# Kernel optimization log

Measured on AMD Instinct MI355X. Metric: run time of the kernel, lower is better.

Reference implementation:

```python
import jax, jax.numpy as jnp
import numpy as np

NC = 6            # CPAB tessellation cells (tess_size=6, zero_boundary=True)
DIM = NC - 1      # theta dimension = 5
SIG_LEN = 2048
CHANNELS = 3
BATCH = 256
FC_IN = 64 * 168  # flattened net_part1 output for signal_len=2048
NUM_SCALING = 0   # N in transform_data_ss
EPS_BN = 1e-5


def _cpab_basis():
    """QR null-space basis of the CPAB continuity + zero-boundary constraints.
    Params ordered [a_1,b_1,...,a_NC,b_NC]; v(x)=a_c x + b_c on cell c."""
    nc = NC
    L = np.zeros((nc + 1, 2 * nc))
    for k in range(1, nc):  # continuity at internal knots x_k = k/nc
        xk = k / nc
        L[k - 1, 2 * (k - 1)] = xk
        L[k - 1, 2 * (k - 1) + 1] = 1.0
        L[k - 1, 2 * k] = -xk
        L[k - 1, 2 * k + 1] = -1.0
    L[nc - 1, 1] = 1.0        # v(0) = 0  -> b_1 = 0
    L[nc, 2 * (nc - 1)] = 1.0  # v(1) = 0 -> a_nc + b_nc = 0
    L[nc, 2 * nc - 1] = 1.0
    Q, _ = np.linalg.qr(L.T, mode='complete')
    return np.ascontiguousarray(Q[:, nc + 1:]).astype(np.float32)  # (12, 5)


def _conv1d(x, w, b):
    y = jax.lax.conv_general_dilated(x, w, (1,), 'VALID',
                                     dimension_numbers=('NCH', 'OIH', 'NCH'))
    return y + b[None, :, None]


def _maxpool1d(x, k, s):
    return jax.lax.reduce_window(x, -jnp.inf, jax.lax.max, (1, 1, k), (1, 1, s), 'VALID')


def _bn(x, g, b, m, v):  # eval-mode BatchNorm1d
    return (x - m[None, :, None]) * (g / jnp.sqrt(v + EPS_BN))[None, :, None] + b[None, :, None]


def _integrate(x, A):
    """Exact CPAB 1D flow integration over t=1 with cell-crossing handling.
    x: (B, n) points in [0,1]; A: (B, NC, 2) per-cell (a, b). Monotone
    trajectories cross at most NC-1 boundaries -> fixed NC+1 iterations."""
    a_all, b_all = A[:, :, 0], A[:, :, 1]
    t = jnp.ones_like(x)
    for _ in range(NC + 1):
        c = jnp.clip(jnp.floor(x * NC).astype(jnp.int32), 0, NC - 1)
        a = jnp.take_along_axis(a_all, c, axis=1)
        b = jnp.take_along_axis(b_all, c, axis=1)
        v = a * x + b
        xb = jnp.where(v >= 0, (c + 1).astype(x.dtype) / NC, c.astype(x.dtype) / NC)
        big_a = jnp.abs(a) > 1e-8
        a_s = jnp.where(big_a, a, 1.0)
        z = x + b / a_s        # shifted coord: x(t) = z*exp(a t) - b/a
        zb = xb + b / a_s
        ratio = zb / jnp.where(jnp.abs(z) > 1e-12, z, 1e-12)
        t_exp = jnp.log(jnp.maximum(ratio, 1e-12)) / a_s
        v_s = jnp.where(jnp.abs(v) > 1e-12, v, 1.0)
        t_lin = (xb - x) / v_s
        thit = jnp.where(big_a, t_exp, t_lin)
        valid = (jnp.abs(v) > 1e-12) & (thit > 0) & (jnp.where(big_a, ratio, 1.0) > 0)
        thit = jnp.where(valid, thit, jnp.inf)
        tau = jnp.minimum(t, thit)
        x_new = jnp.where(big_a, z * jnp.exp(a * tau) - (z - x), x + b * tau)
        hit = thit <= t
        nudge = jnp.where(v >= 0, 1e-6, -1e-6)  # push into next cell
        x = jnp.clip(jnp.where(hit, xb + nudge, x_new), 0.0, 1.0)
        t = jnp.maximum(t - tau, 0.0)
    return x


def _interp1d(data, pos):
    """data: (B, L, C); pos: (B, n) in [0,1] -> (B, n, C) linear interpolation."""
    Lw = data.shape[1]
    p = jnp.clip(pos, 0.0, 1.0) * (Lw - 1)
    x0 = jnp.clip(jnp.floor(p).astype(jnp.int32), 0, Lw - 2)
    w = (p - x0.astype(p.dtype))[:, :, None]
    d0 = jnp.take_along_axis(data, x0[:, :, None], axis=1)
    d1 = jnp.take_along_axis(data, (x0 + 1)[:, :, None], axis=1)
    return d0 * (1.0 - w) + d1 * w


def _transform_data_ss(data, theta, basis, outsize, N):
    """CPAB scaling-and-squaring warp of data (B, L, C) by theta (B, DIM)."""
    Bsz = theta.shape[0]
    A = (theta @ basis.T).reshape(Bsz, NC, 2) / (2.0 ** N)
    grid = jnp.linspace(0.0, 1.0, outsize, dtype=data.dtype)
    grid_t = _integrate(jnp.broadcast_to(grid, (Bsz, outsize)), A)
    for _ in range(N):  # squaring: compose the warp with itself
        grid_t = _interp1d(grid_t[:, :, None], grid_t)[:, :, 0]
    return _interp1d(data, grid_t)


def reference(x, conv1_w, conv1_b, bn1_g, bn1_b, bn1_m, bn1_v,
              conv2_w, conv2_b, bn2_g, bn2_b, bn2_m, bn2_v,
              conv3_w, conv3_b, bn3_g, bn3_b, bn3_m, bn3_v,
              fc1_w, fc1_b, fc2_w, fc2_b, fc3_w, fc3_b, fc4_w, fc4_b, basis):
    # localization net (n_recurrence = 1, back_version = True)
    h = jax.nn.relu(_maxpool1d(_bn(_conv1d(x, conv1_w, conv1_b), bn1_g, bn1_b, bn1_m, bn1_v), 3, 2))
    h = jax.nn.relu(_maxpool1d(_bn(_conv1d(h, conv2_w, conv2_b), bn2_g, bn2_b, bn2_m, bn2_v), 3, 3))
    h = jax.nn.relu(_maxpool1d(_bn(_conv1d(h, conv3_w, conv3_b), bn3_g, bn3_b, bn3_m, bn3_v), 3, 2))
    xs = h.reshape(h.shape[0], -1)  # (B, 64*168)
    xs = jax.nn.relu(xs @ fc1_w.T + fc1_b)
    xs = jax.nn.relu(xs @ fc2_w.T + fc2_b)
    xs = jax.nn.relu(xs @ fc3_w.T + fc3_b)
    theta = jnp.tanh(xs @ fc4_w.T + fc4_b)  # (B, 5)
    data = jnp.transpose(x, (0, 2, 1))       # (B, L, C)
    warped = _transform_data_ss(data, theta, basis, SIG_LEN, NUM_SCALING)
    return jnp.transpose(warped, (0, 2, 1))  # (B, C, L)


def setup_inputs() -> dict:
    key = jax.random.key(0)
    ks = jax.random.split(key, 16)
    def nrm(k, shape, scale):
        return (jax.random.normal(k, shape) * scale).astype(jnp.float32)
    inp = {}
    inp['x'] = jax.random.normal(ks[0], (BATCH, CHANNELS, SIG_LEN), dtype=jnp.float32)
    inp['conv1_w'] = nrm(ks[1], (128, CHANNELS, 3), (CHANNELS * 3) ** -0.5)
    inp['conv1_b'] = nrm(ks[2], (128,), 0.01)
    inp['bn1_g'] = jnp.ones((128,), jnp.float32)
    inp['bn1_b'] = jnp.zeros((128,), jnp.float32)
    inp['bn1_m'] = nrm(ks[3], (128,), 0.1)
    inp['bn1_v'] = jnp.ones((128,), jnp.float32)
    inp['conv2_w'] = nrm(ks[4], (64, 128, 5), (128 * 5) ** -0.5)
    inp['conv2_b'] = nrm(ks[5], (64,), 0.01)
    inp['bn2_g'] = jnp.ones((64,), jnp.float32)
    inp['bn2_b'] = jnp.zeros((64,), jnp.float32)
    inp['bn2_m'] = nrm(ks[6], (64,), 0.1)
    inp['bn2_v'] = jnp.ones((64,), jnp.float32)
    inp['conv3_w'] = nrm(ks[7], (64, 64, 3), (64 * 3) ** -0.5)
    inp['conv3_b'] = nrm(ks[8], (64,), 0.01)
    inp['bn3_g'] = jnp.ones((64,), jnp.float32)
    inp['bn3_b'] = jnp.zeros((64,), jnp.float32)
    inp['bn3_m'] = nrm(ks[9], (64,), 0.1)
    inp['bn3_v'] = jnp.ones((64,), jnp.float32)
    inp['fc1_w'] = nrm(ks[10], (48, FC_IN), FC_IN ** -0.5)
    inp['fc1_b'] = jnp.zeros((48,), jnp.float32)
    inp['fc2_w'] = nrm(ks[11], (32, 48), 48 ** -0.5)
    inp['fc2_b'] = jnp.zeros((32,), jnp.float32)
    inp['fc3_w'] = nrm(ks[12], (16, 32), 32 ** -0.5)
    inp['fc3_b'] = jnp.zeros((16,), jnp.float32)
    # near-identity warp head (original zero-inits weight, identity bias)
    inp['fc4_w'] = nrm(ks[13], (DIM, 16), 0.01)
    inp['fc4_b'] = nrm(ks[14], (DIM,), 0.01)
    inp['basis'] = jnp.asarray(_cpab_basis())
    return inp
```

## Files before the change

### kernel.cpp

```cpp
#include <hip/hip_runtime.h>
#include <math.h>

#define BATCH   256
#define SIGLEN  2048
#define L1OUT   1022
#define L2OUT   339
#define L3OUT   168
#define FCIN    10752

#define TP2   21
#define NROW  68
#define H1S   136
#define H1SZ  (NROW*H1S)

#define TU3   28

#define KC1   12
#define KCL   (FCIN/KC1)

typedef float f32x4  __attribute__((ext_vector_type(4)));
typedef float f32x16 __attribute__((ext_vector_type(16)));
typedef short s16x8  __attribute__((ext_vector_type(8)));

__device__ __forceinline__ unsigned short f2bf(float f) {
    unsigned int u = __float_as_uint(f);
    return (unsigned short)((u + 0x7fffu + ((u >> 16) & 1u)) >> 16);
}
__device__ __forceinline__ float bf2f(unsigned short h) {
    return __uint_as_float(((unsigned int)h) << 16);
}

__launch_bounds__(256)
__global__ void prep_kernel(
    const float* __restrict__ conv1_b,
    const float* __restrict__ g1, const float* __restrict__ b1,
    const float* __restrict__ m1, const float* __restrict__ v1,
    const float* __restrict__ conv2_w, const float* __restrict__ conv2_b,
    const float* __restrict__ g2, const float* __restrict__ b2,
    const float* __restrict__ m2, const float* __restrict__ v2,
    const float* __restrict__ conv3_w, const float* __restrict__ conv3_b,
    const float* __restrict__ g3, const float* __restrict__ b3,
    const float* __restrict__ m3, const float* __restrict__ v3,
    unsigned short* __restrict__ w2hi, unsigned short* __restrict__ w2lo,
    unsigned short* __restrict__ w3hi, unsigned short* __restrict__ w3lo,
    float* __restrict__ so1, float* __restrict__ so2, float* __restrict__ so3)
{
    int tid = blockIdx.x * 256 + threadIdx.x;
    int stride = gridDim.x * 256;
    for (int i = tid; i < 64*128*5; i += stride) {
        int co = i / 640; int rr = i - co*640; int ci = rr / 5; int k = rr - ci*5;
        float w = conv2_w[i];
        unsigned short hi = f2bf(w);
        unsigned short lo = f2bf(w - bf2f(hi));
        int seg = k*8 + (ci >> 4);
        int dst = ((seg*2 + (co >> 5))*32 + (co & 31))*16 + (ci & 15);
        w2hi[dst] = hi;
        w2lo[dst] = lo;
    }
    for (int i = tid; i < 64*64*3; i += stride) {
        int co = i / 192; int r = i - co*192; int ci = r / 3; int k = r - ci*3;
        float w = conv3_w[i];
        unsigned short hi = f2bf(w);
        unsigned short lo = f2bf(w - bf2f(hi));
        int dst = ((k*2 + (ci >> 5))*64 + co)*32 + (ci & 31);
        w3hi[dst] = hi;
        w3lo[dst] = lo;
    }
    if (tid < 128) {
        float s = g1[tid] / sqrtf(v1[tid] + 1e-5f);
        so1[tid]       = s;
        so1[128 + tid] = (conv1_b[tid] - m1[tid]) * s + b1[tid];
    }
    if (tid < 64) {
        float s2 = g2[tid] / sqrtf(v2[tid] + 1e-5f);
        so2[tid]      = s2;
        so2[64 + tid] = (conv2_b[tid] - m2[tid]) * s2 + b2[tid];
        float s3 = g3[tid] / sqrtf(v3[tid] + 1e-5f);
        so3[tid]      = s3;
        so3[64 + tid] = (conv3_b[tid] - m3[tid]) * s3 + b3[tid];
    }
}

__launch_bounds__(256, 4)
__global__ void conv12_kernel(
    const float* __restrict__ x, const float* __restrict__ w1,
    const unsigned short* __restrict__ w2hi, const unsigned short* __restrict__ w2lo,
    const float* __restrict__ so1, const float* __restrict__ so2,
    unsigned int* __restrict__ h2p)
{
    __shared__ unsigned short h1s[2 * H1SZ];

    int t  = threadIdx.x;
    int b  = blockIdx.x;
    int u0 = blockIdx.y * TP2;
    int q0 = 3 * u0;
    int wv = __builtin_amdgcn_readfirstlane(t >> 6);
    int l  = t & 63;

    float wr[2][9];
    float s1r[2], o1r[2];
    #pragma unroll
    for (int h = 0; h < 2; ++h) {
        int ch = l + 64*h;
        #pragma unroll
        for (int j = 0; j < 9; ++j) wr[h][j] = w1[ch*9 + j];
        s1r[h] = so1[ch]; o1r[h] = so1[128 + ch];
    }
    for (int s = 0; s < 17; ++s) {
        int r = 4*s + wv;
        int xbase = 2*(q0 + r);
        float xv[3][5];
        #pragma unroll
        for (int ci = 0; ci < 3; ++ci) {
            const float* xp = x + (b*3 + ci)*SIGLEN;
            #pragma unroll
            for (int d = 0; d < 5; ++d) {
                int xi = xbase + d; xi = xi < SIGLEN ? xi : SIGLEN - 1;
                xv[ci][d] = xp[xi];
            }
        }
        #pragma unroll
        for (int h = 0; h < 2; ++h) {
            float r0 = 0.f, r1 = 0.f, r2 = 0.f;
            #pragma unroll
            for (int ci = 0; ci < 3; ++ci) {
                float wA = wr[h][ci*3], wB = wr[h][ci*3+1], wC = wr[h][ci*3+2];
                r0 = fmaf(xv[ci][0], wA, fmaf(xv[ci][1], wB, fmaf(xv[ci][2], wC, r0)));
                r1 = fmaf(xv[ci][1], wA, fmaf(xv[ci][2], wB, fmaf(xv[ci][3], wC, r1)));
                r2 = fmaf(xv[ci][2], wA, fmaf(xv[ci][3], wB, fmaf(xv[ci][4], wC, r2)));
            }
            float mx = fmaxf(r0, fmaxf(r1, r2));
            float v  = fmaxf(fmaf(s1r[h], mx, o1r[h]), 0.f);
            unsigned short hi = f2bf(v);
            unsigned short lo = f2bf(v - bf2f(hi));
            h1s[r*H1S + l + 64*h]        = hi;
            h1s[H1SZ + r*H1S + l + 64*h] = lo;
        }
    }
    __syncthreads();

    int chf = wv & 1;
    int kh  = wv >> 1;
    int r32 = l & 31;
    int oct = l >> 5;

    f32x16 acc0 = (f32x16)(0.f);
    f32x16 acc1 = (f32x16)(0.f);
    const unsigned short* whB = w2hi + (chf*32 + r32)*16 + oct*8;
    const unsigned short* wlB = w2lo + (chf*32 + r32)*16 + oct*8;

    #pragma unroll 4
    for (int ss = 0; ss < 20; ++ss) {
        int sg = kh*20 + ss;
        int ks = sg >> 3, cb = sg & 7;
        s16x8 wh = *(const s16x8*)(whB + sg*1024);
        s16x8 wl = *(const s16x8*)(wlB + sg*1024);
        int row0 = r32 + ks;
        int row1 = 32 + r32 + ks;
        s16x8 ah0 = *(const s16x8*)&h1s[row0*H1S + cb*16 + oct*8];
        s16x8 al0 = *(const s16x8*)&h1s[H1SZ + row0*H1S + cb*16 + oct*8];
        s16x8 ah1 = *(const s16x8*)&h1s[row1*H1S + cb*16 + oct*8];
        s16x8 al1 = *(const s16x8*)&h1s[H1SZ + row1*H1S + cb*16 + oct*8];
        acc0 = __builtin_amdgcn_mfma_f32_32x32x16_bf16(ah0, wh, acc0, 0, 0, 0);
        acc1 = __builtin_amdgcn_mfma_f32_32x32x16_bf16(ah1, wh, acc1, 0, 0, 0);
        acc0 = __builtin_amdgcn_mfma_f32_32x32x16_bf16(al0, wh, acc0, 0, 0, 0);
        acc1 = __builtin_amdgcn_mfma_f32_32x32x16_bf16(al1, wh, acc1, 0, 0, 0);
        acc0 = __builtin_amdgcn_mfma_f32_32x32x16_bf16(ah0, wl, acc0, 0, 0, 0);
        acc1 = __builtin_amdgcn_mfma_f32_32x32x16_bf16(ah1, wl, acc1, 0, 0, 0);
    }
    __syncthreads();

    float* c2 = (float*)h1s;
    #pragma unroll
    for (int rg = 0; rg < 16; ++rg) {
        int row = (rg & 3) + 8*(rg >> 2) + 4*oct;
        c2[kh*4160 + row*65        + chf*32 + r32] = acc0[rg];
        c2[kh*4160 + (32 + row)*65 + chf*32 + r32] = acc1[rg];
    }
    __syncthreads();

    #pragma unroll
    for (int it = 0; it < 6; ++it) {
        int idx = t + it*256;
        if (idx < TP2*64) {
            int ul = idx >> 6, co = idx & 63;
            int u = u0 + ul;
            if (u < L2OUT) {
                float v0 = c2[(3*ul  )*65 + co] + c2[4160 + (3*ul  )*65 + co];
                float v1 = c2[(3*ul+1)*65 + co] + c2[4160 + (3*ul+1)*65 + co];
                float v2 = c2[(3*ul+2)*65 + co] + c2[4160 + (3*ul+2)*65 + co];
                float mm = fmaxf(v0, fmaxf(v1, v2));
                float v  = fmaxf(fmaf(so2[co], mm, so2[64 + co]), 0.f);
                unsigned short hi = f2bf(v);
                unsigned short lo = f2bf(v - bf2f(hi));
                h2p[(b*L2OUT + u)*64 + co] = (unsigned int)hi | ((unsigned int)lo << 16);
            }
        }
    }
}

__launch_bounds__(256, 4)
__global__ void conv3_kernel(
    const unsigned int* __restrict__ h2p,
    const unsigned short* __restrict__ w3hi, const unsigned short* __restrict__ w3lo,
    const float* __restrict__ so3, float* __restrict__ xs)
{
    __shared__ unsigned short h3hi[66 * 72];
    __shared__ unsigned short h3lo[66 * 72];

    int t  = threadIdx.x;
    int b  = blockIdx.x;
    int u0 = blockIdx.y * TU3;
    int wv = __builtin_amdgcn_readfirstlane(t >> 6);
    int l  = t & 63;
    int m  = l & 15;
    int qd = l >> 4;

    for (int i = t; i < 66*64; i += 256) {
        int r = i >> 6, ci = i & 63;
        int g = 2*u0 + r; g = g > (L2OUT-1) ? (L2OUT-1) : g;
        unsigned int v = h2p[(b*L2OUT + g)*64 + ci];
        h3hi[r*72 + ci] = (unsigned short)(v & 0xffffu);
        h3lo[r*72 + ci] = (unsigned short)(v >> 16);
    }
    __syncthreads();

    s16x8 wh[6], wl[6];
    #pragma unroll
    for (int s = 0; s < 6; ++s) {
        wh[s] = *(const s16x8*)(w3hi + s*2048 + (wv*16 + m)*32 + qd*8);
        wl[s] = *(const s16x8*)(w3lo + s*2048 + (wv*16 + m)*32 + qd*8);
    }

    f32x4 acc[4] = {(f32x4)(0.f), (f32x4)(0.f), (f32x4)(0.f), (f32x4)(0.f)};
    #pragma unroll
    for (int pt = 0; pt < 4; ++pt) {
        #pragma unroll
        for (int s = 0; s < 6; ++s) {
            int row = pt*16 + m + (s >> 1);
            int off = (s & 1)*32 + qd*8;
            s16x8 ah = *(const s16x8*)&h3hi[row*72 + off];
            s16x8 al = *(const s16x8*)&h3lo[row*72 + off];
            acc[pt] = __builtin_amdgcn_mfma_f32_16x16x32_bf16(ah, wh[s], acc[pt], 0, 0, 0);
            acc[pt] = __builtin_amdgcn_mfma_f32_16x16x32_bf16(al, wh[s], acc[pt], 0, 0, 0);
            acc[pt] = __builtin_amdgcn_mfma_f32_16x16x32_bf16(ah, wl[s], acc[pt], 0, 0, 0);
        }
    }
    __syncthreads();

    float* c3 = (float*)h3hi;
    #pragma unroll
    for (int pt = 0; pt < 4; ++pt)
        #pragma unroll
        for (int rg = 0; rg < 4; ++rg)
            c3[(pt*16 + qd*4 + rg)*65 + wv*16 + m] = acc[pt][rg];
    __syncthreads();

    #pragma unroll
    for (int it = 0; it < 7; ++it) {
        int idx = t + it*256;
        if (idx < TU3*64) {
            int co = idx / TU3, ul = idx - co*TU3;
            int p = 2*ul;
            float v0 = c3[(p  )*65 + co];
            float v1 = c3[(p+1)*65 + co];
            float v2 = c3[(p+2)*65 + co];
            float mm = fmaxf(v0, fmaxf(v1, v2));
            xs[b*FCIN + co*L3OUT + (u0 + ul)] = fmaxf(fmaf(so3[co], mm, so3[64 + co]), 0.f);
        }
    }
}

__launch_bounds__(256)
__global__ void fc1_kernel(
    const float* __restrict__ xs, const float* __restrict__ w,
    float* __restrict__ part)
{
    int t = threadIdx.x, lane = t & 63, wid = t >> 6;
    int b0 = blockIdx.x * 4;
    int kc = blockIdx.y;
    int o0 = wid * 12;
    float acc[48];
    #pragma unroll
    for (int i = 0; i < 48; ++i) acc[i] = 0.f;

    int kbase = kc * KCL + lane;
    for (int ki = 0; ki < KCL/64; ++ki) {
        int k = kbase + ki * 64;
        float xv0 = xs[(b0 + 0) * FCIN + k];
        float xv1 = xs[(b0 + 1) * FCIN + k];
        float xv2 = xs[(b0 + 2) * FCIN + k];
        float xv3 = xs[(b0 + 3) * FCIN + k];
        #pragma unroll
        for (int j = 0; j < 12; ++j) {
            float ww = w[(o0 + j) * FCIN + k];
            acc[j]      += xv0 * ww;
            acc[12 + j] += xv1 * ww;
            acc[24 + j] += xv2 * ww;
            acc[36 + j] += xv3 * ww;
        }
    }
    #pragma unroll
    for (int i = 0; i < 48; ++i) {
        #pragma unroll
        for (int off = 32; off > 0; off >>= 1)
            acc[i] += __shfl_xor(acc[i], off, 64);
    }
    if (lane == 0) {
        #pragma unroll
        for (int bb = 0; bb < 4; ++bb)
            #pragma unroll
            for (int j = 0; j < 12; ++j)
                part[((b0 + bb) * 48 + o0 + j) * KC1 + kc] = acc[bb * 12 + j];
    }
}

__launch_bounds__(256)
__global__ void warp_kernel(
    const float* __restrict__ x, const float* __restrict__ part,
    const float* __restrict__ fc1_b,
    const float* __restrict__ fc2_w, const float* __restrict__ fc2_b,
    const float* __restrict__ fc3_w, const float* __restrict__ fc3_b,
    const float* __restrict__ fc4_w, const float* __restrict__ fc4_b,
    const float* __restrict__ basis,
    float* __restrict__ out)
{
    __shared__ float xsl[48];
    __shared__ float hl[32];
    __shared__ float gl[16];
    __shared__ float thl[5];
    __shared__ float Al[12];

    int b = blockIdx.x;
    int t = threadIdx.x;

    if (t < 48) {
        const float4* p = (const float4*)&part[(b * 48 + t) * KC1];
        float4 pa = p[0], pb = p[1], pc = p[2];
        float sv = ((pa.x + pa.y) + (pa.z + pa.w))
                 + ((pb.x + pb.y) + (pb.z + pb.w))
                 + ((pc.x + pc.y) + (pc.z + pc.w));
        xsl[t] = fmaxf(sv + fc1_b[t], 0.f);
    }
    __syncthreads();
    if (t < 32) {
        float sv = fc2_b[t];
        #pragma unroll
        for (int k = 0; k < 48; ++k) sv = fmaf(fc2_w[t * 48 + k], xsl[k], sv);
        hl[t] = fmaxf(sv, 0.f);
    }
    __syncthreads();
    if (t < 16) {
        float sv = fc3_b[t];
        #pragma unroll
        for (int k = 0; k < 32; ++k) sv = fmaf(fc3_w[t * 32 + k], hl[k], sv);
        gl[t] = fmaxf(sv, 0.f);
    }
    __syncthreads();
    if (t < 5) {
        float sv = fc4_b[t];
        #pragma unroll
        for (int k = 0; k < 16; ++k) sv = fmaf(fc4_w[t * 16 + k], gl[k], sv);
        thl[t] = tanhf(sv);
    }
    __syncthreads();
    if (t < 12) {
        float sv = 0.f;
        #pragma unroll
        for (int d = 0; d < 5; ++d) sv = fmaf(basis[t * 5 + d], thl[d], sv);
        Al[t] = sv;
    }
    __syncthreads();

    float a_r[6], b_r[6];
    #pragma unroll
    for (int c = 0; c < 6; ++c) { a_r[c] = Al[2*c]; b_r[c] = Al[2*c+1]; }

    for (int ch = 0; ch < 8; ++ch) {
        int i = ch * 256 + t;
        float xp = (float)i / 2047.f;
        float tt = 1.f;
        for (int it = 0; it < 7; ++it) {
            int c = (int)floorf(xp * 6.f);
            c = min(max(c, 0), 5);
            float a  = a_r[c], bb = b_r[c];
            float v  = a * xp + bb;
            float xb = (v >= 0.f) ? (float)(c + 1) / 6.f : (float)c / 6.f;
            bool  big_a = fabsf(a) > 1e-8f;
            float a_s = big_a ? a : 1.f;
            float z   = xp + bb / a_s;
            float zb  = xb + bb / a_s;
            float zden = (fabsf(z) > 1e-12f) ? z : 1e-12f;
            float ratio = zb / zden;
            float t_exp = logf(fmaxf(ratio, 1e-12f)) / a_s;
            float v_s   = (fabsf(v) > 1e-12f) ? v : 1.f;
            float t_lin = (xb - xp) / v_s;
            float thit  = big_a ? t_exp : t_lin;
            bool valid  = (fabsf(v) > 1e-12f) && (thit > 0.f) && ((big_a ? ratio : 1.f) > 0.f);
            if (!valid) thit = __builtin_inff();
            float tau   = fminf(tt, thit);
            float x_new = big_a ? (z * expf(a * tau) - (z - xp)) : (xp + bb * tau);
            bool hit    = (thit <= tt);
            float nudge = (v >= 0.f) ? 1e-6f : -1e-6f;
            xp = hit ? (xb + nudge) : x_new;
            xp = fminf(fmaxf(xp, 0.f), 1.f);
            tt = fmaxf(tt - tau, 0.f);
        }
        float p = fminf(fmaxf(xp, 0.f), 1.f) * 2047.f;
        int i0 = (int)floorf(p);
        i0 = min(max(i0, 0), 2046);
        float w = p - (float)i0;
        #pragma unroll
        for (int c = 0; c < 3; ++c) {
            const float* d = &x[(b * 3 + c) * SIGLEN];
            out[(b * 3 + c) * SIGLEN + i] = d[i0] * (1.f - w) + d[i0 + 1] * w;
        }
    }
}

extern "C" void kernel_launch(void* const* d_in, const int* in_sizes, int n_in,
                              void* d_out, int out_size, void* d_ws, size_t ws_size,
                              hipStream_t stream) {
    (void)in_sizes; (void)n_in; (void)out_size; (void)ws_size;
    const float* x       = (const float*)d_in[0];
    const float* conv1_w = (const float*)d_in[1];
    const float* conv1_b = (const float*)d_in[2];
    const float* bn1_g   = (const float*)d_in[3];
    const float* bn1_b   = (const float*)d_in[4];
    const float* bn1_m   = (const float*)d_in[5];
    const float* bn1_v   = (const float*)d_in[6];
    const float* conv2_w = (const float*)d_in[7];
    const float* conv2_b = (const float*)d_in[8];
    const float* bn2_g   = (const float*)d_in[9];
    const float* bn2_b   = (const float*)d_in[10];
    const float* bn2_m   = (const float*)d_in[11];
    const float* bn2_v   = (const float*)d_in[12];
    const float* conv3_w = (const float*)d_in[13];
    const float* conv3_b = (const float*)d_in[14];
    const float* bn3_g   = (const float*)d_in[15];
    const float* bn3_b   = (const float*)d_in[16];
    const float* bn3_m   = (const float*)d_in[17];
    const float* bn3_v   = (const float*)d_in[18];
    const float* fc1_w   = (const float*)d_in[19];
    const float* fc1_b   = (const float*)d_in[20];
    const float* fc2_w   = (const float*)d_in[21];
    const float* fc2_b   = (const float*)d_in[22];
    const float* fc3_w   = (const float*)d_in[23];
    const float* fc3_b   = (const float*)d_in[24];
    const float* fc4_w   = (const float*)d_in[25];
    const float* fc4_b   = (const float*)d_in[26];
    const float* basis   = (const float*)d_in[27];

    unsigned short* w2hi = (unsigned short*)d_ws;
    unsigned short* w2lo = w2hi + 40960;
    unsigned short* w3hi = w2lo + 40960;
    unsigned short* w3lo = w3hi + 12288;
    float* ws   = (float*)d_ws;
    float* so1  = ws + 53248;
    float* so2  = so1 + 256;
    float* so3  = so2 + 128;
    unsigned int* h2p = (unsigned int*)(so3 + 128);
    float* xs   = (float*)(h2p + 5554176);
    float* part = xs + 2752512;

    prep_kernel<<<64, 256, 0, stream>>>(
        conv1_b, bn1_g, bn1_b, bn1_m, bn1_v,
        conv2_w, conv2_b, bn2_g, bn2_b, bn2_m, bn2_v,
        conv3_w, conv3_b, bn3_g, bn3_b, bn3_m, bn3_v,
        w2hi, w2lo, w3hi, w3lo, so1, so2, so3);

    dim3 g2(BATCH, (L2OUT + TP2 - 1) / TP2);
    conv12_kernel<<<g2, 256, 0, stream>>>(x, conv1_w, w2hi, w2lo, so1, so2, h2p);

    dim3 g3(BATCH, L3OUT / TU3);
    conv3_kernel<<<g3, 256, 0, stream>>>(h2p, w3hi, w3lo, so3, xs);

    dim3 gfc(BATCH / 4, KC1);
    fc1_kernel<<<gfc, 256, 0, stream>>>(xs, fc1_w, part);

    warp_kernel<<<BATCH, 256, 0, stream>>>(x, part, fc1_b, fc2_w, fc2_b,
                                           fc3_w, fc3_b, fc4_w, fc4_b, basis,
                                           (float*)d_out);
}
```

Measured before the change: 268.4 us.

## Fuse conv3, fc1 and warp into a single per-sample tail kernel

Merges conv3, fc1 and the CPAB warp kernel into one kernel with one block per sample. The conv3 output stays in shared memory (about 43 KB), so the xs round trip through global memory, the split-K partials and two launches go away. In exchange, each block loops serially over six conv3 tiles, the grid drops to 256 blocks, and fc1 weights are reloaded once per sample rather than shared across four samples. The larger shared-memory footprint also limits occupancy.

```diff
diff --git a/kernel.cpp b/kernel.cpp
--- a/kernel.cpp
+++ b/kernel.cpp
@@ -14,9 +14,6 @@
 #define H1SZ  (NROW*H1S)
 
 #define TU3   28
-
-#define KC1   12
-#define KCL   (FCIN/KC1)
 
 typedef float f32x4  __attribute__((ext_vector_type(4)));
 typedef float f32x16 __attribute__((ext_vector_type(16)));
@@ -199,154 +196,119 @@
     }
 }
 
-__launch_bounds__(256, 4)
-__global__ void conv3_kernel(
+__launch_bounds__(256)
+__global__ void tail_kernel(
     const unsigned int* __restrict__ h2p,
     const unsigned short* __restrict__ w3hi, const unsigned short* __restrict__ w3lo,
-    const float* __restrict__ so3, float* __restrict__ xs)
-{
-    __shared__ unsigned short h3hi[66 * 72];
-    __shared__ unsigned short h3lo[66 * 72];
-
-    int t  = threadIdx.x;
-    int b  = blockIdx.x;
-    int u0 = blockIdx.y * TU3;
-    int wv = __builtin_amdgcn_readfirstlane(t >> 6);
-    int l  = t & 63;
-    int m  = l & 15;
-    int qd = l >> 4;
-
-    for (int i = t; i < 66*64; i += 256) {
-        int r = i >> 6, ci = i & 63;
-        int g = 2*u0 + r; g = g > (L2OUT-1) ? (L2OUT-1) : g;
-        unsigned int v = h2p[(b*L2OUT + g)*64 + ci];
-        h3hi[r*72 + ci] = (unsigned short)(v & 0xffffu);
-        h3lo[r*72 + ci] = (unsigned short)(v >> 16);
-    }
-    __syncthreads();
-
-    s16x8 wh[6], wl[6];
-    #pragma unroll
-    for (int s = 0; s < 6; ++s) {
-        wh[s] = *(const s16x8*)(w3hi + s*2048 + (wv*16 + m)*32 + qd*8);
-        wl[s] = *(const s16x8*)(w3lo + s*2048 + (wv*16 + m)*32 + qd*8);
-    }
-
-    f32x4 acc[4] = {(f32x4)(0.f), (f32x4)(0.f), (f32x4)(0.f), (f32x4)(0.f)};
-    #pragma unroll
-    for (int pt = 0; pt < 4; ++pt) {
-        #pragma unroll
-        for (int s = 0; s < 6; ++s) {
-            int row = pt*16 + m + (s >> 1);
-            int off = (s & 1)*32 + qd*8;
-            s16x8 ah = *(const s16x8*)&h3hi[row*72 + off];
-            s16x8 al = *(const s16x8*)&h3lo[row*72 + off];
-            acc[pt] = __builtin_amdgcn_mfma_f32_16x16x32_bf16(ah, wh[s], acc[pt], 0, 0, 0);
-            acc[pt] = __builtin_amdgcn_mfma_f32_16x16x32_bf16(al, wh[s], acc[pt], 0, 0, 0);
-            acc[pt] = __builtin_amdgcn_mfma_f32_16x16x32_bf16(ah, wl[s], acc[pt], 0, 0, 0);
-        }
-    }
-    __syncthreads();
-
-    float* c3 = (float*)h3hi;
-    #pragma unroll
-    for (int pt = 0; pt < 4; ++pt)
-        #pragma unroll
-        for (int rg = 0; rg < 4; ++rg)
-            c3[(pt*16 + qd*4 + rg)*65 + wv*16 + m] = acc[pt][rg];
-    __syncthreads();
-
-    #pragma unroll
-    for (int it = 0; it < 7; ++it) {
-        int idx = t + it*256;
-        if (idx < TU3*64) {
-            int co = idx / TU3, ul = idx - co*TU3;
-            int p = 2*ul;
-            float v0 = c3[(p  )*65 + co];
-            float v1 = c3[(p+1)*65 + co];
-            float v2 = c3[(p+2)*65 + co];
-            float mm = fmaxf(v0, fmaxf(v1, v2));
-            xs[b*FCIN + co*L3OUT + (u0 + ul)] = fmaxf(fmaf(so3[co], mm, so3[64 + co]), 0.f);
-        }
-    }
-}
-
-__launch_bounds__(256)
-__global__ void fc1_kernel(
-    const float* __restrict__ xs, const float* __restrict__ w,
-    float* __restrict__ part)
-{
-    int t = threadIdx.x, lane = t & 63, wid = t >> 6;
-    int b0 = blockIdx.x * 4;
-    int kc = blockIdx.y;
-    int o0 = wid * 12;
-    float acc[48];
-    #pragma unroll
-    for (int i = 0; i < 48; ++i) acc[i] = 0.f;
-
-    int kbase = kc * KCL + lane;
-    for (int ki = 0; ki < KCL/64; ++ki) {
-        int k = kbase + ki * 64;
-        float xv0 = xs[(b0 + 0) * FCIN + k];
-        float xv1 = xs[(b0 + 1) * FCIN + k];
-        float xv2 = xs[(b0 + 2) * FCIN + k];
-        float xv3 = xs[(b0 + 3) * FCIN + k];
-        #pragma unroll
-        for (int j = 0; j < 12; ++j) {
-            float ww = w[(o0 + j) * FCIN + k];
-            acc[j]      += xv0 * ww;
-            acc[12 + j] += xv1 * ww;
-            acc[24 + j] += xv2 * ww;
-            acc[36 + j] += xv3 * ww;
-        }
-    }
-    #pragma unroll
-    for (int i = 0; i < 48; ++i) {
-        #pragma unroll
-        for (int off = 32; off > 0; off >>= 1)
-            acc[i] += __shfl_xor(acc[i], off, 64);
-    }
-    if (lane == 0) {
-        #pragma unroll
-        for (int bb = 0; bb < 4; ++bb)
-            #pragma unroll
-            for (int j = 0; j < 12; ++j)
-                part[((b0 + bb) * 48 + o0 + j) * KC1 + kc] = acc[bb * 12 + j];
-    }
-}
-
-__launch_bounds__(256)
-__global__ void warp_kernel(
-    const float* __restrict__ x, const float* __restrict__ part,
-    const float* __restrict__ fc1_b,
+    const float* __restrict__ so3,
+    const float* __restrict__ x,
+    const float* __restrict__ fc1_w, const float* __restrict__ fc1_b,
     const float* __restrict__ fc2_w, const float* __restrict__ fc2_b,
     const float* __restrict__ fc3_w, const float* __restrict__ fc3_b,
     const float* __restrict__ fc4_w, const float* __restrict__ fc4_b,
     const float* __restrict__ basis,
     float* __restrict__ out)
 {
-    __shared__ float xsl[48];
-    __shared__ float hl[32];
-    __shared__ float gl[16];
-    __shared__ float thl[5];
-    __shared__ float Al[12];
-
-    int b = blockIdx.x;
-    int t = threadIdx.x;
-
-    if (t < 48) {
-        const float4* p = (const float4*)&part[(b * 48 + t) * KC1];
-        float4 pa = p[0], pb = p[1], pc = p[2];
-        float sv = ((pa.x + pa.y) + (pa.z + pa.w))
-                 + ((pb.x + pb.y) + (pb.z + pb.w))
-                 + ((pc.x + pc.y) + (pc.z + pc.w));
-        xsl[t] = fmaxf(sv + fc1_b[t], 0.f);
-    }
-    __syncthreads();
+    __shared__ float xsl[FCIN];
+    __shared__ unsigned short h3s[2*66*72];
+    __shared__ float c3buf[64*65];
+    __shared__ float xs48[48], hl[32], gl[16], thl[5], Al[12];
+
+    int t  = threadIdx.x;
+    int b  = blockIdx.x;
+    int wv = __builtin_amdgcn_readfirstlane(t >> 6);
+    int l  = t & 63;
+    int m  = l & 15;
+    int qd = l >> 4;
+
+    s16x8 wh[6], wl[6];
+    #pragma unroll
+    for (int s = 0; s < 6; ++s) {
+        wh[s] = *(const s16x8*)(w3hi + s*2048 + (wv*16 + m)*32 + qd*8);
+        wl[s] = *(const s16x8*)(w3lo + s*2048 + (wv*16 + m)*32 + qd*8);
+    }
+    float s3a = so3[t & 63], s3b = so3[64 + (t & 63)];
+
+    for (int ti = 0; ti < 6; ++ti) {
+        int u0 = ti * TU3;
+        for (int i = t; i < 66*64; i += 256) {
+            int r = i >> 6, ci = i & 63;
+            int g = 2*u0 + r; g = g > (L2OUT-1) ? (L2OUT-1) : g;
+            unsigned int v = h2p[(b*L2OUT + g)*64 + ci];
+            h3s[r*72 + ci]          = (unsigned short)(v & 0xffffu);
+            h3s[66*72 + r*72 + ci]  = (unsigned short)(v >> 16);
+        }
+        __syncthreads();
+
+        f32x4 acc[4] = {(f32x4)(0.f), (f32x4)(0.f), (f32x4)(0.f), (f32x4)(0.f)};
+        #pragma unroll
+        for (int pt = 0; pt < 4; ++pt) {
+            #pragma unroll
+            for (int s = 0; s < 6; ++s) {
+                int row = pt*16 + m + (s >> 1);
+                int off = (s & 1)*32 + qd*8;
+                s16x8 ah = *(const s16x8*)&h3s[row*72 + off];
+                s16x8 al = *(const s16x8*)&h3s[66*72 + row*72 + off];
+                acc[pt] = __builtin_amdgcn_mfma_f32_16x16x32_bf16(ah, wh[s], acc[pt], 0, 0, 0);
+                acc[pt] = __builtin_amdgcn_mfma_f32_16x16x32_bf16(al, wh[s], acc[pt], 0, 0, 0);
+                acc[pt] = __builtin_amdgcn_mfma_f32_16x16x32_bf16(ah, wl[s], acc[pt], 0, 0, 0);
+            }
+        }
+        #pragma unroll
+        for (int pt = 0; pt < 4; ++pt)
+            #pragma unroll
+            for (int rg = 0; rg < 4; ++rg)
+                c3buf[(pt*16 + qd*4 + rg)*65 + wv*16 + m] = acc[pt][rg];
+        __syncthreads();
+
+        #pragma unroll
+        for (int it = 0; it < 7; ++it) {
+            int idx = t + it*256;
+            if (idx < TU3*64) {
+                int co = idx / TU3, ul = idx - co*TU3;
+                int p = 2*ul;
+                float v0 = c3buf[(p  )*65 + co];
+                float v1 = c3buf[(p+1)*65 + co];
+                float v2 = c3buf[(p+2)*65 + co];
+                float mm = fmaxf(v0, fmaxf(v1, v2));
+                xsl[co*L3OUT + u0 + ul] = fmaxf(fmaf(so3[co], mm, so3[64 + co]), 0.f);
+            }
+        }
+        __syncthreads();
+    }
+
+    {
+        int o0 = wv * 12;
+        float acc[12];
+        #pragma unroll
+        for (int j = 0; j < 12; ++j) acc[j] = 0.f;
+        for (int ki = 0; ki < 42; ++ki) {
+            int k4 = (ki*64 + l) * 4;
+            float4 xv = *(const float4*)&xsl[k4];
+            #pragma unroll
+            for (int j = 0; j < 12; ++j) {
+                float4 wv4 = *(const float4*)&fc1_w[(o0 + j)*FCIN + k4];
+                acc[j] = fmaf(xv.x, wv4.x, fmaf(xv.y, wv4.y, fmaf(xv.z, wv4.z, fmaf(xv.w, wv4.w, acc[j]))));
+            }
+        }
+        #pragma unroll
+        for (int j = 0; j < 12; ++j) {
+            #pragma unroll
+            for (int off = 32; off > 0; off >>= 1)
+                acc[j] += __shfl_xor(acc[j], off, 64);
+        }
+        if (l == 0) {
+            #pragma unroll
+            for (int j = 0; j < 12; ++j)
+                xs48[o0 + j] = fmaxf(acc[j] + fc1_b[o0 + j], 0.f);
+        }
+    }
+    __syncthreads();
+
     if (t < 32) {
         float sv = fc2_b[t];
         #pragma unroll
-        for (int k = 0; k < 48; ++k) sv = fmaf(fc2_w[t * 48 + k], xsl[k], sv);
+        for (int k = 0; k < 48; ++k) sv = fmaf(fc2_w[t * 48 + k], xs48[k], sv);
         hl[t] = fmaxf(sv, 0.f);
     }
     __syncthreads();
@@ -416,6 +378,7 @@
             out[(b * 3 + c) * SIGLEN + i] = d[i0] * (1.f - w) + d[i0 + 1] * w;
         }
     }
+    (void)s3a; (void)s3b;
 }
 
 extern "C" void kernel_launch(void* const* d_in, const int* in_sizes, int n_in,
@@ -460,8 +423,6 @@
     float* so2  = so1 + 256;
     float* so3  = so2 + 128;
     unsigned int* h2p = (unsigned int*)(so3 + 128);
-    float* xs   = (float*)(h2p + 5554176);
-    float* part = xs + 2752512;
 
     prep_kernel<<<64, 256, 0, stream>>>(
         conv1_b, bn1_g, bn1_b, bn1_m, bn1_v,
@@ -472,13 +433,8 @@
     dim3 g2(BATCH, (L2OUT + TP2 - 1) / TP2);
     conv12_kernel<<<g2, 256, 0, stream>>>(x, conv1_w, w2hi, w2lo, so1, so2, h2p);
 
-    dim3 g3(BATCH, L3OUT / TU3);
-    conv3_kernel<<<g3, 256, 0, stream>>>(h2p, w3hi, w3lo, so3, xs);
-
-    dim3 gfc(BATCH / 4, KC1);
-    fc1_kernel<<<gfc, 256, 0, stream>>>(xs, fc1_w, part);
-
-    warp_kernel<<<BATCH, 256, 0, stream>>>(x, part, fc1_b, fc2_w, fc2_b,
+    tail_kernel<<<BATCH, 256, 0, stream>>>(h2p, w3hi, w3lo, so3, x,
+                                           fc1_w, fc1_b, fc2_w, fc2_b,
                                            fc3_w, fc3_b, fc4_w, fc4_b, basis,
                                            (float*)d_out);
 }
```

New measurement: 279.6 us. 1.04x slower.

## Switch conv2 MFMA from 32x32x16 split-K to 16x16x32 per-wave channel tiles

Applied to the files above, without the earlier changes.

Conv2 now uses 16x16x32 bf16 MFMAs. Each wave owns 16 output channels across all 64 rows and the full K range, instead of splitting K across two wave pairs with 32x32 tiles. The weight layout in prep is reorganized to match, and the hi/lo activation buffers are split into separate shared arrays. This drops the split-K partial-sum buffer and the extra addition in the pooling epilogue. In exchange each wave issues more, smaller MFMAs and does more LDS loads for activations.

```diff
diff --git a/kernel.cpp b/kernel.cpp
--- a/kernel.cpp
+++ b/kernel.cpp
@@ -19,7 +19,6 @@
 #define KCL   (FCIN/KC1)
 
 typedef float f32x4  __attribute__((ext_vector_type(4)));
-typedef float f32x16 __attribute__((ext_vector_type(16)));
 typedef short s16x8  __attribute__((ext_vector_type(8)));
 
 __device__ __forceinline__ unsigned short f2bf(float f) {
@@ -52,8 +51,7 @@
         float w = conv2_w[i];
         unsigned short hi = f2bf(w);
         unsigned short lo = f2bf(w - bf2f(hi));
-        int seg = k*8 + (ci >> 4);
-        int dst = ((seg*2 + (co >> 5))*32 + (co & 31))*16 + (ci & 15);
+        int dst = ((k*4 + (ci >> 5))*64 + co)*32 + (ci & 31);
         w2hi[dst] = hi;
         w2lo[dst] = lo;
     }
@@ -88,7 +86,8 @@
     const float* __restrict__ so1, const float* __restrict__ so2,
     unsigned int* __restrict__ h2p)
 {
-    __shared__ unsigned short h1s[2 * H1SZ];
+    __shared__ unsigned short h1hi[H1SZ];
+    __shared__ unsigned short h1lo[H1SZ];
 
     int t  = threadIdx.x;
     int b  = blockIdx.x;
@@ -96,6 +95,8 @@
     int q0 = 3 * u0;
     int wv = __builtin_amdgcn_readfirstlane(t >> 6);
     int l  = t & 63;
+    int m  = l & 15;
+    int qd = l >> 4;
 
     float wr[2][9];
     float s1r[2], o1r[2];
@@ -133,50 +134,42 @@
             float v  = fmaxf(fmaf(s1r[h], mx, o1r[h]), 0.f);
             unsigned short hi = f2bf(v);
             unsigned short lo = f2bf(v - bf2f(hi));
-            h1s[r*H1S + l + 64*h]        = hi;
-            h1s[H1SZ + r*H1S + l + 64*h] = lo;
-        }
-    }
-    __syncthreads();
-
-    int chf = wv & 1;
-    int kh  = wv >> 1;
-    int r32 = l & 31;
-    int oct = l >> 5;
-
-    f32x16 acc0 = (f32x16)(0.f);
-    f32x16 acc1 = (f32x16)(0.f);
-    const unsigned short* whB = w2hi + (chf*32 + r32)*16 + oct*8;
-    const unsigned short* wlB = w2lo + (chf*32 + r32)*16 + oct*8;
-
-    #pragma unroll 4
-    for (int ss = 0; ss < 20; ++ss) {
-        int sg = kh*20 + ss;
-        int ks = sg >> 3, cb = sg & 7;
-        s16x8 wh = *(const s16x8*)(whB + sg*1024);
-        s16x8 wl = *(const s16x8*)(wlB + sg*1024);
-        int row0 = r32 + ks;
-        int row1 = 32 + r32 + ks;
-        s16x8 ah0 = *(const s16x8*)&h1s[row0*H1S + cb*16 + oct*8];
-        s16x8 al0 = *(const s16x8*)&h1s[H1SZ + row0*H1S + cb*16 + oct*8];
-        s16x8 ah1 = *(const s16x8*)&h1s[row1*H1S + cb*16 + oct*8];
-        s16x8 al1 = *(const s16x8*)&h1s[H1SZ + row1*H1S + cb*16 + oct*8];
-        acc0 = __builtin_amdgcn_mfma_f32_32x32x16_bf16(ah0, wh, acc0, 0, 0, 0);
-        acc1 = __builtin_amdgcn_mfma_f32_32x32x16_bf16(ah1, wh, acc1, 0, 0, 0);
-        acc0 = __builtin_amdgcn_mfma_f32_32x32x16_bf16(al0, wh, acc0, 0, 0, 0);
-        acc1 = __builtin_amdgcn_mfma_f32_32x32x16_bf16(al1, wh, acc1, 0, 0, 0);
-        acc0 = __builtin_amdgcn_mfma_f32_32x32x16_bf16(ah0, wl, acc0, 0, 0, 0);
-        acc1 = __builtin_amdgcn_mfma_f32_32x32x16_bf16(ah1, wl, acc1, 0, 0, 0);
-    }
-    __syncthreads();
-
-    float* c2 = (float*)h1s;
-    #pragma unroll
-    for (int rg = 0; rg < 16; ++rg) {
-        int row = (rg & 3) + 8*(rg >> 2) + 4*oct;
-        c2[kh*4160 + row*65        + chf*32 + r32] = acc0[rg];
-        c2[kh*4160 + (32 + row)*65 + chf*32 + r32] = acc1[rg];
-    }
+            h1hi[r*H1S + l + 64*h] = hi;
+            h1lo[r*H1S + l + 64*h] = lo;
+        }
+    }
+    __syncthreads();
+
+    f32x4 acc[4] = {(f32x4)(0.f), (f32x4)(0.f), (f32x4)(0.f), (f32x4)(0.f)};
+
+    const unsigned short* whb = w2hi + wv*512 + m*32 + qd*8;
+    const unsigned short* wlb = w2lo + wv*512 + m*32 + qd*8;
+
+    for (int k = 0; k < 5; ++k) {
+        #pragma unroll
+        for (int cb = 0; cb < 4; ++cb) {
+            int st = k*4 + cb;
+            s16x8 wh = *(const s16x8*)(whb + st*2048);
+            s16x8 wl = *(const s16x8*)(wlb + st*2048);
+            #pragma unroll
+            for (int pt = 0; pt < 4; ++pt) {
+                int row = pt*16 + m + k;
+                s16x8 ah = *(const s16x8*)&h1hi[row*H1S + cb*32 + qd*8];
+                s16x8 al = *(const s16x8*)&h1lo[row*H1S + cb*32 + qd*8];
+                acc[pt] = __builtin_amdgcn_mfma_f32_16x16x32_bf16(ah, wh, acc[pt], 0, 0, 0);
+                acc[pt] = __builtin_amdgcn_mfma_f32_16x16x32_bf16(al, wh, acc[pt], 0, 0, 0);
+                acc[pt] = __builtin_amdgcn_mfma_f32_16x16x32_bf16(ah, wl, acc[pt], 0, 0, 0);
+            }
+        }
+    }
+    __syncthreads();
+
+    float* c2 = (float*)h1hi;
+    #pragma unroll
+    for (int pt = 0; pt < 4; ++pt)
+        #pragma unroll
+        for (int rg = 0; rg < 4; ++rg)
+            c2[(pt*16 + qd*4 + rg)*65 + wv*16 + m] = acc[pt][rg];
     __syncthreads();
 
     #pragma unroll
@@ -186,9 +179,9 @@
             int ul = idx >> 6, co = idx & 63;
             int u = u0 + ul;
             if (u < L2OUT) {
-                float v0 = c2[(3*ul  )*65 + co] + c2[4160 + (3*ul  )*65 + co];
-                float v1 = c2[(3*ul+1)*65 + co] + c2[4160 + (3*ul+1)*65 + co];
-                float v2 = c2[(3*ul+2)*65 + co] + c2[4160 + (3*ul+2)*65 + co];
+                float v0 = c2[(3*ul  )*65 + co];
+                float v1 = c2[(3*ul+1)*65 + co];
+                float v2 = c2[(3*ul+2)*65 + co];
                 float mm = fmaxf(v0, fmaxf(v1, v2));
                 float v  = fmaxf(fmaf(so2[co], mm, so2[64 + co]), 0.f);
                 unsigned short hi = f2bf(v);
@@ -325,11 +318,7 @@
     const float* __restrict__ basis,
     float* __restrict__ out)
 {
-    __shared__ float xsl[48];
-    __shared__ float hl[32];
-    __shared__ float gl[16];
-    __shared__ float thl[5];
-    __shared__ float Al[12];
+    __shared__ float xs48[48], hl[32], gl[16], thl[5], Al[12];
 
     int b = blockIdx.x;
     int t = threadIdx.x;
@@ -340,13 +329,13 @@
         float sv = ((pa.x + pa.y) + (pa.z + pa.w))
                  + ((pb.x + pb.y) + (pb.z + pb.w))
                  + ((pc.x + pc.y) + (pc.z + pc.w));
-        xsl[t] = fmaxf(sv + fc1_b[t], 0.f);
+        xs48[t] = fmaxf(sv + fc1_b[t], 0.f);
     }
     __syncthreads();
     if (t < 32) {
         float sv = fc2_b[t];
         #pragma unroll
-        for (int k = 0; k < 48; ++k) sv = fmaf(fc2_w[t * 48 + k], xsl[k], sv);
+        for (int k = 0; k < 48; ++k) sv = fmaf(fc2_w[t * 48 + k], xs48[k], sv);
         hl[t] = fmaxf(sv, 0.f);
     }
     __syncthreads();
```

After: 256.2 us. 1.05x faster.
